# Optimization experiments

Hardware: AMD Instinct MI355X
Metric: run time of the kernel (lower is better)

The kernel has to match this reference:

```python
import jax, jax.numpy as jnp
import numpy as np
from itertools import combinations

B, M = 128, 24
EMB = 16
NEG_SLOPE = 0.01  # torch F.leaky_relu default


def _combo_index():
    # 60 combinations: choose 2 of 4 hole cards x choose 3 of 5 board cards.
    hero = list(combinations(range(4), 2))      # 6
    board = list(combinations(range(5), 3))     # 10
    combos = []
    for h in hero:
        for b in board:
            combos.append([h[0], h[1], 4 + b[0], 4 + b[1], 4 + b[2]])
    return np.asarray(combos, dtype=np.int32)   # (60, 5)

_COMBOS = jnp.asarray(_combo_index())


def setup_inputs() -> dict:
    key = jax.random.key(0)
    ks = jax.random.split(key, 12)
    ranks = jax.random.randint(ks[0], (B, M, 9), 1, 14)   # 1..13
    suits = jax.random.randint(ks[1], (B, M, 9), 1, 5)    # 1..4
    x = jnp.stack([ranks, suits], axis=-1).reshape(B, M, 18).astype(jnp.int64)

    def lin(k, fan_in, fan_out):
        bound = 1.0 / np.sqrt(fan_in)
        kw, kb = jax.random.split(k)
        W = jax.random.uniform(kw, (fan_in, fan_out), minval=-bound, maxval=bound, dtype=jnp.float32)
        b = jax.random.uniform(kb, (fan_out,), minval=-bound, maxval=bound, dtype=jnp.float32)
        return W, b

    card_emb = jax.random.normal(ks[2], (53, EMB), dtype=jnp.float32)
    card_emb = card_emb.at[0].set(0.0)  # padding_idx=0
    hand_W, hand_b = lin(ks[3], 32, 128)
    board_W, board_b = lin(ks[4], 48, 128)
    hidden_W, hidden_b = lin(ks[5], 256, 256)
    out_W, out_b = lin(ks[6], 60 * 256, 256)
    return {"x": x, "card_emb": card_emb,
            "hand_W": hand_W, "hand_b": hand_b,
            "board_W": board_W, "board_b": board_b,
            "hidden_W": hidden_W, "hidden_b": hidden_b,
            "out_W": out_W, "out_b": out_b}


def reference(x, card_emb, hand_W, hand_b, board_W, board_b,
              hidden_W, hidden_b, out_W, out_b):
    act = lambda v: jax.nn.leaky_relu(v, NEG_SLOPE)
    Bx, Mx = x.shape[0], x.shape[1]
    ranks = x[..., 0::2]                       # (B,M,9)
    suits = x[..., 1::2]
    rc = jnp.take(ranks, _COMBOS, axis=-1)     # (B,M,60,5)
    sc = jnp.take(suits, _COMBOS, axis=-1)
    rc = jnp.where(rc > 0, rc - 1, 0)          # ranks -> 0..12
    sc = jnp.where(sc > 0, (sc - 1) * 13, 0)   # suit offset 0/13/26/39
    cards = rc + sc                            # (B,M,60,5) in [0,52)
    emb = card_emb[cards]                      # (B,M,60,5,16)
    hero = emb[..., :2, :].reshape(Bx, Mx, 60, 32)
    board = emb[..., 2:, :].reshape(Bx, Mx, 60, 48)
    hero = act(hero @ hand_W + hand_b)         # (B,M,60,128)
    board = act(board @ board_W + board_b)     # (B,M,60,128)
    h = act(jnp.concatenate([hero, board], axis=-1) @ hidden_W + hidden_b)  # (B,M,60,256)
    flat = h.reshape(Bx, Mx, 60 * 256)         # (B,M,15360)
    return act(flat @ out_W + out_b)           # (B,M,256)
```

## Files before the change

### kernel.cpp

```cpp
#include <hip/hip_runtime.h>
#include <hip/hip_bf16.h>
#include <cstdint>
#include <cstddef>

typedef __hip_bfloat16 bf16;
typedef __attribute__((ext_vector_type(8))) short short8;
typedef __attribute__((ext_vector_type(4))) float floatx4;

#define KO 15360
#define KS 16
#define KSLICE 960
#define NIT (KSLICE / 64)

__device__ __forceinline__ float lrelu(float v) { return v > 0.f ? v : 0.01f * v; }

__device__ __forceinline__ float bflo(unsigned int u) {
  unsigned int x = u << 16; float f; __builtin_memcpy(&f, &x, 4); return f;
}
__device__ __forceinline__ float bfhi(unsigned int u) {
  unsigned int x = u & 0xffff0000u; float f; __builtin_memcpy(&f, &x, 4); return f;
}
__device__ __forceinline__ unsigned int pk2(float lo, float hi) {
  bf16 a = __float2bfloat16(lo), b = __float2bfloat16(hi);
  unsigned short ua, ub;
  __builtin_memcpy(&ua, &a, 2); __builtin_memcpy(&ub, &b, 2);
  return (unsigned int)ua | ((unsigned int)ub << 16);
}
__device__ __forceinline__ unsigned int hpair(unsigned int u, unsigned int v) {
  return pk2(lrelu(bflo(u) + bflo(v)), lrelu(bfhi(u) + bfhi(v)));
}

__device__ __forceinline__ void async_lds16(const bf16* g, bf16* l) {
  __builtin_amdgcn_global_load_lds((__attribute__((address_space(1))) void*)(g),
                                   (__attribute__((address_space(3))) void*)(l),
                                   16, 0, 0);
}

__global__ __launch_bounds__(256) void transpose_k(const float* __restrict__ W,
                                                   bf16* __restrict__ Wt, int K)
{
  __shared__ float tile[64][65];
  const int kb = blockIdx.x * 64;
  const int nb = blockIdx.y * 64;
  const int t = threadIdx.x;
  #pragma unroll
  for (int i = 0; i < 16; ++i) {
    int idx = t + 256 * i;
    int r = idx >> 6, c = idx & 63;
    tile[r][c] = W[(size_t)(kb + r) * 256 + nb + c];
  }
  __syncthreads();
  #pragma unroll
  for (int i = 0; i < 16; ++i) {
    int idx = t + 256 * i;
    int r = idx >> 6, c = idx & 63;
    Wt[(size_t)(nb + r) * K + kb + c] = __float2bfloat16(tile[c][r]);
  }
}

__global__ __launch_bounds__(256) void pack_hidden(const float* __restrict__ W,
                                                   bf16* __restrict__ P)
{
  __shared__ float Lt[4096];
  const int g = blockIdx.x, t = threadIdx.x;
  for (int i = t; i < 4096; i += 256)
    Lt[i] = W[(size_t)(i >> 4) * 256 + g * 16 + (i & 15)];
  __syncthreads();
  #pragma unroll
  for (int cc = 0; cc < 2; ++cc) {
    int c = t + 256 * cc;
    int ks = c >> 6, l = c & 63, lr = l & 15, quad = l >> 4;
    short8 v;
    #pragma unroll
    for (int j = 0; j < 8; ++j) {
      bf16 b = __float2bfloat16(Lt[(ks * 32 + quad * 8 + j) * 16 + lr]);
      short s; __builtin_memcpy(&s, &b, 2);
      v[j] = s;
    }
    *(short8*)(P + ((size_t)(g * 8 + ks) * 64 + l) * 8) = v;
  }
}

__global__ __launch_bounds__(256) void hb_pack(
    const int* __restrict__ x, const float* __restrict__ card_emb,
    const float* __restrict__ hand_W, const float* __restrict__ hand_b,
    const float* __restrict__ board_W, const float* __restrict__ board_b,
    bf16* __restrict__ Abuf)
{
  static constexpr int H0[6] = {0,0,0,1,1,2};
  static constexpr int H1[6] = {1,2,3,2,3,3};
  static constexpr int B0[10] = {0,0,0,0,0,0,1,1,1,2};
  static constexpr int B1[10] = {1,1,1,2,2,3,2,2,3,3};
  static constexpr int B2[10] = {2,3,4,3,4,4,3,4,4,4};

  __shared__ float wH[32 * 128];
  __shared__ float wB[48 * 128];
  __shared__ float bH[128], bB[128];
  __shared__ float emb[4][9][16];
  __shared__ bf16 At[2][16][264];

  const int t = threadIdx.x;
  const int item0 = blockIdx.x * 4;

  for (int i = t * 4; i < 4096; i += 1024) *(float4*)&wH[i] = *(const float4*)&hand_W[i];
  for (int i = t * 4; i < 6144; i += 1024) *(float4*)&wB[i] = *(const float4*)&board_W[i];
  if (t < 128) { bH[t] = hand_b[t]; bB[t] = board_b[t]; }
  for (int ii = t; ii < 576; ii += 256) {
    int li = ii / 144, idx = ii - li * 144;
    int ci = idx >> 4, e = idx & 15;
    int rk = x[(item0 + li) * 18 + 2 * ci], st = x[(item0 + li) * 18 + 2 * ci + 1];
    int card = (rk > 0 ? rk - 1 : 0) + (st > 0 ? (st - 1) * 13 : 0);
    emb[li][ci][e] = card_emb[card * 16 + e];
  }
  __syncthreads();

  const int half = t >> 7, j = t & 127;

  for (int pass = 0; pass < 2; ++pass) {
    if (pass) __syncthreads();
    const int embi = 2 * pass + half;
    {
      bf16 z = __float2bfloat16(0.f);
      #pragma unroll
      for (int p = 0; p < 6; ++p) At[half][p][128 + j] = z;
      #pragma unroll
      for (int b = 0; b < 10; ++b) At[half][6 + b][j] = z;
    }
    float aH[6], aB[10];
    {
      float hb = bH[j], bb = bB[j];
      #pragma unroll
      for (int p = 0; p < 6; ++p) aH[p] = hb;
      #pragma unroll
      for (int b = 0; b < 10; ++b) aB[b] = bb;
    }
    #pragma unroll
    for (int k = 0; k < 16; ++k) {
      float e[9];
      #pragma unroll
      for (int c = 0; c < 9; ++c) e[c] = emb[embi][c][k];
      float w0 = wH[k * 128 + j], w1 = wH[(16 + k) * 128 + j];
      float v0 = wB[k * 128 + j], v1 = wB[(16 + k) * 128 + j], v2 = wB[(32 + k) * 128 + j];
      #pragma unroll
      for (int p = 0; p < 6; ++p)
        aH[p] += e[H0[p]] * w0 + e[H1[p]] * w1;
      #pragma unroll
      for (int b = 0; b < 10; ++b)
        aB[b] += e[4 + B0[b]] * v0 + e[4 + B1[b]] * v1 + e[4 + B2[b]] * v2;
    }
    #pragma unroll
    for (int p = 0; p < 6; ++p) At[half][p][j] = __float2bfloat16(lrelu(aH[p]));
    #pragma unroll
    for (int b = 0; b < 10; ++b) At[half][6 + b][128 + j] = __float2bfloat16(lrelu(aB[b]));
    __syncthreads();

    #pragma unroll
    for (int li2 = 0; li2 < 2; ++li2) {
      #pragma unroll
      for (int cc = 0; cc < 2; ++cc) {
        int c = t + 256 * cc;
        int m = c & 15, kq = (c >> 4) & 3, ks = c >> 6;
        short8 v = *(const short8*)&At[li2][m][ks * 32 + kq * 8];
        *(short8*)(Abuf + (size_t)(item0 + 2 * pass + li2) * 4096 + (size_t)c * 8) = v;
      }
    }
    __syncthreads();
  }
}

__global__ __launch_bounds__(256, 2) void uv_gemm(
    const bf16* __restrict__ Abuf, const bf16* __restrict__ hWtp,
    const float* __restrict__ hidden_b, bf16* __restrict__ UV)
{
  const int t = threadIdx.x, w = t >> 6, l = t & 63;
  const int lr = l & 15, quad = l >> 4;

  short8 bfrag[4][8];
  float bias[4];
  #pragma unroll
  for (int tl = 0; tl < 4; ++tl) {
    bias[tl] = hidden_b[w * 64 + tl * 16 + lr];
    #pragma unroll
    for (int ks = 0; ks < 8; ++ks)
      bfrag[tl][ks] = *(const short8*)(hWtp + ((size_t)((w * 4 + tl) * 8 + ks) * 64 + l) * 8);
  }

  const int i0 = blockIdx.x * 6;
  for (int ii = 0; ii < 6; ++ii) {
    const bf16* ab = Abuf + (size_t)(i0 + ii) * 4096;
    short8 a[8];
    #pragma unroll
    for (int ks = 0; ks < 8; ++ks)
      a[ks] = *(const short8*)(ab + (size_t)(ks * 64 + l) * 8);

    floatx4 acc[4];
    floatx4 zero = {0.f, 0.f, 0.f, 0.f};
    #pragma unroll
    for (int i = 0; i < 4; ++i) acc[i] = zero;
    #pragma unroll
    for (int ks = 0; ks < 8; ++ks)
      #pragma unroll
      for (int tl = 0; tl < 4; ++tl)
        acc[tl] = __builtin_amdgcn_mfma_f32_16x16x32_bf16(a[ks], bfrag[tl][ks], acc[tl], 0, 0, 0);

    bf16* dst = UV + (size_t)(i0 + ii) * 4096;
    #pragma unroll
    for (int tl = 0; tl < 4; ++tl) {
      int n = w * 64 + tl * 16 + lr;
      #pragma unroll
      for (int r = 0; r < 4; ++r) {
        int m = quad * 4 + r;
        float v = acc[tl][r] + (m >= 6 ? bias[tl] : 0.f);
        dst[m * 256 + n] = __float2bfloat16(v);
      }
    }
  }
}

__device__ __forceinline__ void uv_fetch(const bf16* __restrict__ UV, int m0, int ar,
                                         int ac, int ks0, int it,
                                         uint4& u0, uint4& u1, uint4& v0, uint4& v1)
{
  const int gk = ks0 + it * 64;
  const int combo = gk >> 8;
  const int urow = combo / 10, vrow = 6 + (combo - urow * 10);
  const int c0 = gk & 255;
  const bf16* ub = UV + ((size_t)(m0 + ar) * 16 + urow) * 256 + c0 + ac * 16;
  const bf16* vb = UV + ((size_t)(m0 + ar) * 16 + vrow) * 256 + c0 + ac * 16;
  u0 = *(const uint4*)ub;  u1 = *(const uint4*)(ub + 8);
  v0 = *(const uint4*)vb;  v1 = *(const uint4*)(vb + 8);
}

__global__ __launch_bounds__(256, 2) void out_gemm(
    const bf16* __restrict__ UV, const bf16* __restrict__ Wt,
    float* __restrict__ pbuf)
{
  __shared__ bf16 As[64 * 64];
  __shared__ bf16 Bs[256 * 64];

  const int t = threadIdx.x;
  const int id = blockIdx.x;
  const int by = ((id & 7) << 1) | ((id >> 3) & 1);
  const int bx = id >> 4;
  const int w = t >> 6, l = t & 63, lr = l & 15, quad = l >> 4;
  const int m0 = bx * 64;
  const int ks0 = by * KSLICE;
  const int ar = t >> 2, ac = t & 3;

  const bf16* rowp[8];
  {
    int rl = l >> 3, j = (l & 7) ^ rl;
    #pragma unroll
    for (int q = 0; q < 8; ++q)
      rowp[q] = Wt + (size_t)(w * 64 + 8 * q + rl) * KO + ks0 + j * 8;
  }
  bf16* BsW = &Bs[w * 4096];

  floatx4 acc[16];
  floatx4 zero = {0.f, 0.f, 0.f, 0.f};
  #pragma unroll
  for (int i = 0; i < 16; ++i) acc[i] = zero;

  uint4 cu0, cu1, cv0, cv1;
  uv_fetch(UV, m0, ar, ac, ks0, 0, cu0, cu1, cv0, cv1);

  for (int it = 0; it < NIT; ++it) {
    __syncthreads();

    #pragma unroll
    for (int q = 0; q < 8; ++q)
      async_lds16(rowp[q] + it * 64, BsW + q * 512);

    {
      uint4 h0, h1;
      h0.x = hpair(cu0.x, cv0.x); h0.y = hpair(cu0.y, cv0.y);
      h0.z = hpair(cu0.z, cv0.z); h0.w = hpair(cu0.w, cv0.w);
      h1.x = hpair(cu1.x, cv1.x); h1.y = hpair(cu1.y, cv1.y);
      h1.z = hpair(cu1.z, cv1.z); h1.w = hpair(cu1.w, cv1.w);
      int jA0 = (2 * ac) ^ (ar & 7);
      int jA1 = (2 * ac + 1) ^ (ar & 7);
      *(uint4*)&As[ar * 64 + jA0 * 8] = h0;
      *(uint4*)&As[ar * 64 + jA1 * 8] = h1;
    }

    __syncthreads();

    if (it + 1 < NIT)
      uv_fetch(UV, m0, ar, ac, ks0, it + 1, cu0, cu1, cv0, cv1);

    #pragma unroll
    for (int ks = 0; ks < 2; ++ks) {
      short8 af[4], bfr[4];
      #pragma unroll
      for (int i = 0; i < 4; ++i) {
        int row = i * 16 + lr;
        int jp = (4 * ks + quad) ^ (row & 7);
        af[i] = *(const short8*)&As[row * 64 + jp * 8];
      }
      #pragma unroll
      for (int j = 0; j < 4; ++j) {
        int row = w * 64 + j * 16 + lr;
        int jp = (4 * ks + quad) ^ (row & 7);
        bfr[j] = *(const short8*)&Bs[row * 64 + jp * 8];
      }
      #pragma unroll
      for (int i = 0; i < 4; ++i)
        #pragma unroll
        for (int j = 0; j < 4; ++j)
          acc[i * 4 + j] = __builtin_amdgcn_mfma_f32_16x16x32_bf16(af[i], bfr[j], acc[i * 4 + j], 0, 0, 0);
    }
  }

  float* dst = pbuf + (((size_t)by * 48 + bx) * 4 + w) * 4096 + l;
  #pragma unroll
  for (int a = 0; a < 16; ++a)
    #pragma unroll
    for (int r = 0; r < 4; ++r)
      dst[(a * 4 + r) * 64] = acc[a][r];
}

__global__ __launch_bounds__(256) void reduce_bias(
    const float* __restrict__ pbuf, const float* __restrict__ outb,
    float* __restrict__ out, int slice_stride)
{
  int i4 = blockIdx.x * 256 + threadIdx.x;
  int idx = i4 * 4;
  float4 s = *(const float4*)&pbuf[idx];
  #pragma unroll
  for (int k = 1; k < KS; ++k) {
    float4 v = *(const float4*)&pbuf[idx + (size_t)k * slice_stride];
    s.x += v.x; s.y += v.y; s.z += v.z; s.w += v.w;
  }
  int l = idx & 63, q = (idx >> 6) & 63, w2 = (idx >> 12) & 3, bx = idx >> 14;
  int a = q >> 2, r = q & 3, i = a >> 2, tl = a & 3;
  int lr = l & 15, quad = l >> 4;
  int m = bx * 64 + i * 16 + quad * 4 + r;
  int n = w2 * 64 + tl * 16 + lr;
  float4 b = *(const float4*)&outb[n];
  float4 rr;
  rr.x = lrelu(s.x + b.x); rr.y = lrelu(s.y + b.y);
  rr.z = lrelu(s.z + b.z); rr.w = lrelu(s.w + b.w);
  *(float4*)&out[(size_t)m * 256 + n] = rr;
}

extern "C" void kernel_launch(void* const* d_in, const int* in_sizes, int n_in,
                              void* d_out, int out_size, void* d_ws, size_t ws_size,
                              hipStream_t stream)
{
  const int*   x        = (const int*)  d_in[0];
  const float* card_emb = (const float*)d_in[1];
  const float* hand_W   = (const float*)d_in[2];
  const float* hand_b   = (const float*)d_in[3];
  const float* board_W  = (const float*)d_in[4];
  const float* board_b  = (const float*)d_in[5];
  const float* hidden_W = (const float*)d_in[6];
  const float* hidden_b = (const float*)d_in[7];
  const float* out_W    = (const float*)d_in[8];
  const float* out_b    = (const float*)d_in[9];
  float* out = (float*)d_out;

  const int NI = in_sizes[0] / 18;

  char* ws = (char*)d_ws;
  bf16* hWtp = (bf16*)ws;
  bf16* oWt  = (bf16*)(ws + 131072);
  bf16* UV   = (bf16*)(ws + 131072 + 7864320);
  bf16* Abuf = (bf16*)(ws + 131072 + 7864320 + (size_t)NI * 8192);
  float* pbuf = (float*)Abuf;

  pack_hidden<<<16, 256, 0, stream>>>(hidden_W, hWtp);
  transpose_k<<<dim3(240, 4), 256, 0, stream>>>(out_W, oWt, KO);
  hb_pack<<<NI / 4, 256, 0, stream>>>(x, card_emb, hand_W, hand_b,
                                      board_W, board_b, Abuf);
  uv_gemm<<<NI / 6, 256, 0, stream>>>(Abuf, hWtp, hidden_b, UV);
  out_gemm<<<NI / 64 * KS, 256, 0, stream>>>(UV, oWt, pbuf);
  reduce_bias<<<NI / 4, 256, 0, stream>>>(pbuf, out_b, out, NI * 256);
}
```

Measured before the change: 170.6 us.

## Fuse hand/board embedding stage with hidden GEMM and merge weight-prep kernels

Merges the hidden-weight packing and out_W transpose into one launch split by block index. Fuses the hand/board projection stage with the hidden-layer MFMA GEMM, so the activations stay in LDS and are fed straight to MFMA instead of going through a global Abuf round trip. Each block now handles 6 items in 3 passes. This removes two kernel launches and one global write/read of the intermediate, but the fused kernel uses more registers and LDS, which may lower occupancy.

```diff
diff --git a/kernel.cpp b/kernel.cpp
--- a/kernel.cpp
+++ b/kernel.cpp
@@ -36,56 +36,60 @@
                                    16, 0, 0);
 }
 
-__global__ __launch_bounds__(256) void transpose_k(const float* __restrict__ W,
-                                                   bf16* __restrict__ Wt, int K)
-{
-  __shared__ float tile[64][65];
-  const int kb = blockIdx.x * 64;
-  const int nb = blockIdx.y * 64;
+__global__ __launch_bounds__(256) void prep(
+    const float* __restrict__ hidden_W, bf16* __restrict__ hWtp,
+    const float* __restrict__ out_W, bf16* __restrict__ oWt)
+{
+  __shared__ float sbuf[64 * 65];
   const int t = threadIdx.x;
-  #pragma unroll
-  for (int i = 0; i < 16; ++i) {
-    int idx = t + 256 * i;
-    int r = idx >> 6, c = idx & 63;
-    tile[r][c] = W[(size_t)(kb + r) * 256 + nb + c];
-  }
-  __syncthreads();
-  #pragma unroll
-  for (int i = 0; i < 16; ++i) {
-    int idx = t + 256 * i;
-    int r = idx >> 6, c = idx & 63;
-    Wt[(size_t)(nb + r) * K + kb + c] = __float2bfloat16(tile[c][r]);
-  }
-}
-
-__global__ __launch_bounds__(256) void pack_hidden(const float* __restrict__ W,
-                                                   bf16* __restrict__ P)
-{
-  __shared__ float Lt[4096];
-  const int g = blockIdx.x, t = threadIdx.x;
-  for (int i = t; i < 4096; i += 256)
-    Lt[i] = W[(size_t)(i >> 4) * 256 + g * 16 + (i & 15)];
-  __syncthreads();
-  #pragma unroll
-  for (int cc = 0; cc < 2; ++cc) {
-    int c = t + 256 * cc;
-    int ks = c >> 6, l = c & 63, lr = l & 15, quad = l >> 4;
-    short8 v;
-    #pragma unroll
-    for (int j = 0; j < 8; ++j) {
-      bf16 b = __float2bfloat16(Lt[(ks * 32 + quad * 8 + j) * 16 + lr]);
-      short s; __builtin_memcpy(&s, &b, 2);
-      v[j] = s;
-    }
-    *(short8*)(P + ((size_t)(g * 8 + ks) * 64 + l) * 8) = v;
-  }
-}
-
-__global__ __launch_bounds__(256) void hb_pack(
+  const int id = blockIdx.x;
+
+  if (id < 16) {
+    const int g = id;
+    float* Lt = sbuf;
+    for (int i = t; i < 4096; i += 256)
+      Lt[i] = hidden_W[(size_t)(i >> 4) * 256 + g * 16 + (i & 15)];
+    __syncthreads();
+    #pragma unroll
+    for (int cc = 0; cc < 2; ++cc) {
+      int c = t + 256 * cc;
+      int ks = c >> 6, l = c & 63, lr = l & 15, quad = l >> 4;
+      short8 v;
+      #pragma unroll
+      for (int j = 0; j < 8; ++j) {
+        bf16 b = __float2bfloat16(Lt[(ks * 32 + quad * 8 + j) * 16 + lr]);
+        short s; __builtin_memcpy(&s, &b, 2);
+        v[j] = s;
+      }
+      *(short8*)(hWtp + ((size_t)(g * 8 + ks) * 64 + l) * 8) = v;
+    }
+  } else {
+    const int id2 = id - 16;
+    const int kb = (id2 % 240) * 64;
+    const int nb = (id2 / 240) * 64;
+    float (*tile)[65] = (float(*)[65])sbuf;
+    #pragma unroll
+    for (int i = 0; i < 16; ++i) {
+      int idx = t + 256 * i;
+      int r = idx >> 6, c = idx & 63;
+      tile[r][c] = out_W[(size_t)(kb + r) * 256 + nb + c];
+    }
+    __syncthreads();
+    #pragma unroll
+    for (int i = 0; i < 16; ++i) {
+      int idx = t + 256 * i;
+      int r = idx >> 6, c = idx & 63;
+      oWt[(size_t)(nb + r) * KO + kb + c] = __float2bfloat16(tile[c][r]);
+    }
+  }
+}
+
+__global__ __launch_bounds__(256, 2) void hb_uv(
     const int* __restrict__ x, const float* __restrict__ card_emb,
     const float* __restrict__ hand_W, const float* __restrict__ hand_b,
     const float* __restrict__ board_W, const float* __restrict__ board_b,
-    bf16* __restrict__ Abuf)
+    const bf16* __restrict__ hWtp, const float* __restrict__ hidden_b,
+    bf16* __restrict__ UV)
 {
   static constexpr int H0[6] = {0,0,0,1,1,2};
   static constexpr int H1[6] = {1,2,3,2,3,3};
@@ -96,16 +100,17 @@
   __shared__ float wH[32 * 128];
   __shared__ float wB[48 * 128];
   __shared__ float bH[128], bB[128];
-  __shared__ float emb[4][9][16];
+  __shared__ float emb[6][9][16];
   __shared__ bf16 At[2][16][264];
 
   const int t = threadIdx.x;
-  const int item0 = blockIdx.x * 4;
+  const int w = t >> 6, l = t & 63, lr = l & 15, quad = l >> 4;
+  const int item0 = blockIdx.x * 6;
 
   for (int i = t * 4; i < 4096; i += 1024) *(float4*)&wH[i] = *(const float4*)&hand_W[i];
   for (int i = t * 4; i < 6144; i += 1024) *(float4*)&wB[i] = *(const float4*)&board_W[i];
   if (t < 128) { bH[t] = hand_b[t]; bB[t] = board_b[t]; }
-  for (int ii = t; ii < 576; ii += 256) {
+  for (int ii = t; ii < 864; ii += 256) {
     int li = ii / 144, idx = ii - li * 144;
     int ci = idx >> 4, e = idx & 15;
     int rk = x[(item0 + li) * 18 + 2 * ci], st = x[(item0 + li) * 18 + 2 * ci + 1];
@@ -114,67 +119,6 @@
   }
   __syncthreads();
 
-  const int half = t >> 7, j = t & 127;
-
-  for (int pass = 0; pass < 2; ++pass) {
-    if (pass) __syncthreads();
-    const int embi = 2 * pass + half;
-    {
-      bf16 z = __float2bfloat16(0.f);
-      #pragma unroll
-      for (int p = 0; p < 6; ++p) At[half][p][128 + j] = z;
-      #pragma unroll
-      for (int b = 0; b < 10; ++b) At[half][6 + b][j] = z;
-    }
-    float aH[6], aB[10];
-    {
-      float hb = bH[j], bb = bB[j];
-      #pragma unroll
-      for (int p = 0; p < 6; ++p) aH[p] = hb;
-      #pragma unroll
-      for (int b = 0; b < 10; ++b) aB[b] = bb;
-    }
-    #pragma unroll
-    for (int k = 0; k < 16; ++k) {
-      float e[9];
-      #pragma unroll
-      for (int c = 0; c < 9; ++c) e[c] = emb[embi][c][k];
-      float w0 = wH[k * 128 + j], w1 = wH[(16 + k) * 128 + j];
-      float v0 = wB[k * 128 + j], v1 = wB[(16 + k) * 128 + j], v2 = wB[(32 + k) * 128 + j];
-      #pragma unroll
-      for (int p = 0; p < 6; ++p)
-        aH[p] += e[H0[p]] * w0 + e[H1[p]] * w1;
-      #pragma unroll
-      for (int b = 0; b < 10; ++b)
-        aB[b] += e[4 + B0[b]] * v0 + e[4 + B1[b]] * v1 + e[4 + B2[b]] * v2;
-    }
-    #pragma unroll
-    for (int p = 0; p < 6; ++p) At[half][p][j] = __float2bfloat16(lrelu(aH[p]));
-    #pragma unroll
-    for (int b = 0; b < 10; ++b) At[half][6 + b][128 + j] = __float2bfloat16(lrelu(aB[b]));
-    __syncthreads();
-
-    #pragma unroll
-    for (int li2 = 0; li2 < 2; ++li2) {
-      #pragma unroll
-      for (int cc = 0; cc < 2; ++cc) {
-        int c = t + 256 * cc;
-        int m = c & 15, kq = (c >> 4) & 3, ks = c >> 6;
-        short8 v = *(const short8*)&At[li2][m][ks * 32 + kq * 8];
-        *(short8*)(Abuf + (size_t)(item0 + 2 * pass + li2) * 4096 + (size_t)c * 8) = v;
-      }
-    }
-    __syncthreads();
-  }
-}
-
-__global__ __launch_bounds__(256, 2) void uv_gemm(
-    const bf16* __restrict__ Abuf, const bf16* __restrict__ hWtp,
-    const float* __restrict__ hidden_b, bf16* __restrict__ UV)
-{
-  const int t = threadIdx.x, w = t >> 6, l = t & 63;
-  const int lr = l & 15, quad = l >> 4;
-
   short8 bfrag[4][8];
   float bias[4];
   #pragma unroll
@@ -185,33 +129,73 @@
       bfrag[tl][ks] = *(const short8*)(hWtp + ((size_t)((w * 4 + tl) * 8 + ks) * 64 + l) * 8);
   }
 
-  const int i0 = blockIdx.x * 6;
-  for (int ii = 0; ii < 6; ++ii) {
-    const bf16* ab = Abuf + (size_t)(i0 + ii) * 4096;
-    short8 a[8];
-    #pragma unroll
-    for (int ks = 0; ks < 8; ++ks)
-      a[ks] = *(const short8*)(ab + (size_t)(ks * 64 + l) * 8);
-
-    floatx4 acc[4];
-    floatx4 zero = {0.f, 0.f, 0.f, 0.f};
-    #pragma unroll
-    for (int i = 0; i < 4; ++i) acc[i] = zero;
-    #pragma unroll
-    for (int ks = 0; ks < 8; ++ks)
-      #pragma unroll
-      for (int tl = 0; tl < 4; ++tl)
-        acc[tl] = __builtin_amdgcn_mfma_f32_16x16x32_bf16(a[ks], bfrag[tl][ks], acc[tl], 0, 0, 0);
-
-    bf16* dst = UV + (size_t)(i0 + ii) * 4096;
-    #pragma unroll
-    for (int tl = 0; tl < 4; ++tl) {
-      int n = w * 64 + tl * 16 + lr;
-      #pragma unroll
-      for (int r = 0; r < 4; ++r) {
-        int m = quad * 4 + r;
-        float v = acc[tl][r] + (m >= 6 ? bias[tl] : 0.f);
-        dst[m * 256 + n] = __float2bfloat16(v);
+  const int half = t >> 7, j = t & 127;
+
+  for (int pass = 0; pass < 3; ++pass) {
+    if (pass) __syncthreads();
+    const int embi = 2 * pass + half;
+    {
+      bf16 z = __float2bfloat16(0.f);
+      #pragma unroll
+      for (int p = 0; p < 6; ++p) At[half][p][128 + j] = z;
+      #pragma unroll
+      for (int b = 0; b < 10; ++b) At[half][6 + b][j] = z;
+    }
+    float aH[6], aB[10];
+    {
+      float hb = bH[j], bb = bB[j];
+      #pragma unroll
+      for (int p = 0; p < 6; ++p) aH[p] = hb;
+      #pragma unroll
+      for (int b = 0; b < 10; ++b) aB[b] = bb;
+    }
+    #pragma unroll
+    for (int k = 0; k < 16; ++k) {
+      float e[9];
+      #pragma unroll
+      for (int c = 0; c < 9; ++c) e[c] = emb[embi][c][k];
+      float w0 = wH[k * 128 + j], w1 = wH[(16 + k) * 128 + j];
+      float v0 = wB[k * 128 + j], v1 = wB[(16 + k) * 128 + j], v2 = wB[(32 + k) * 128 + j];
+      #pragma unroll
+      for (int p = 0; p < 6; ++p)
+        aH[p] += e[H0[p]] * w0 + e[H1[p]] * w1;
+      #pragma unroll
+      for (int b = 0; b < 10; ++b)
+        aB[b] += e[4 + B0[b]] * v0 + e[4 + B1[b]] * v1 + e[4 + B2[b]] * v2;
+    }
+    #pragma unroll
+    for (int p = 0; p < 6; ++p) At[half][p][j] = __float2bfloat16(lrelu(aH[p]));
+    #pragma unroll
+    for (int b = 0; b < 10; ++b) At[half][6 + b][128 + j] = __float2bfloat16(lrelu(aB[b]));
+    __syncthreads();
+
+    #pragma unroll
+    for (int li = 0; li < 2; ++li) {
+      short8 a[8];
+      #pragma unroll
+      for (int ks = 0; ks < 8; ++ks)
+        a[ks] = *(const short8*)&At[li][lr][ks * 32 + quad * 8];
+
+      floatx4 acc[4];
+      floatx4 zero = {0.f, 0.f, 0.f, 0.f};
+      #pragma unroll
+      for (int i = 0; i < 4; ++i) acc[i] = zero;
+      #pragma unroll
+      for (int ks = 0; ks < 8; ++ks)
+        #pragma unroll
+        for (int tl = 0; tl < 4; ++tl)
+          acc[tl] = __builtin_amdgcn_mfma_f32_16x16x32_bf16(a[ks], bfrag[tl][ks], acc[tl], 0, 0, 0);
+
+      bf16* dst = UV + (size_t)(item0 + 2 * pass + li) * 4096;
+      #pragma unroll
+      for (int tl = 0; tl < 4; ++tl) {
+        int n = w * 64 + tl * 16 + lr;
+        #pragma unroll
+        for (int r = 0; r < 4; ++r) {
+          int m = quad * 4 + r;
+          float v = acc[tl][r] + (m >= 6 ? bias[tl] : 0.f);
+          dst[m * 256 + n] = __float2bfloat16(v);
+        }
       }
     }
   }
@@ -365,14 +349,11 @@
   bf16* hWtp = (bf16*)ws;
   bf16* oWt  = (bf16*)(ws + 131072);
   bf16* UV   = (bf16*)(ws + 131072 + 7864320);
-  bf16* Abuf = (bf16*)(ws + 131072 + 7864320 + (size_t)NI * 8192);
-  float* pbuf = (float*)Abuf;
-
-  pack_hidden<<<16, 256, 0, stream>>>(hidden_W, hWtp);
-  transpose_k<<<dim3(240, 4), 256, 0, stream>>>(out_W, oWt, KO);
-  hb_pack<<<NI / 4, 256, 0, stream>>>(x, card_emb, hand_W, hand_b,
-                                      board_W, board_b, Abuf);
-  uv_gemm<<<NI / 6, 256, 0, stream>>>(Abuf, hWtp, hidden_b, UV);
+  float* pbuf = (float*)(ws + 131072 + 7864320 + (size_t)NI * 8192);
+
+  prep<<<16 + 240 * 4, 256, 0, stream>>>(hidden_W, hWtp, out_W, oWt);
+  hb_uv<<<NI / 6, 256, 0, stream>>>(x, card_emb, hand_W, hand_b,
+                                    board_W, board_b, hWtp, hidden_b, UV);
   out_gemm<<<NI / 64 * KS, 256, 0, stream>>>(UV, oWt, pbuf);
   reduce_bias<<<NI / 4, 256, 0, stream>>>(pbuf, out_b, out, NI * 256);
 }
```

After: 185.0 us. 8.5% more time.
